# Kernel tuning notes

Hardware: AMD Instinct MI355X
Metric: run time of the kernel (lower is better)

The kernel has to match this reference:

```python
import jax, jax.numpy as jnp
import numpy as np

D, H, DFF = 1024, 16, 4096
B, T, S = 2, 2048, 2048
DK = D // H
EPS = 1e-5


def _linear(x, W, b):
    # torch nn.Linear: x @ W.T + b
    return jnp.einsum('bsd,od->bso', x, W) + b


def _mha(q_in, k_in, v_in, mask, Wq, bq, Wk, bk, Wv, bv, Wo, bo):
    Bq = q_in.shape[0]
    Q = _linear(q_in, Wq, bq).reshape(Bq, -1, H, DK)
    K = _linear(k_in, Wk, bk).reshape(Bq, -1, H, DK)
    V = _linear(v_in, Wv, bv).reshape(Bq, -1, H, DK)
    scores = jnp.einsum('bqhd,bkhd->bhqk', Q, K) / jnp.sqrt(jnp.float32(DK))
    if mask is not None:
        scores = jnp.where(mask[:, None, :, :] == 0, jnp.float32(-1e9), scores)
    attn = jax.nn.softmax(scores, axis=-1)
    ctx = jnp.einsum('bhqk,bkhd->bqhd', attn, V).reshape(Bq, -1, D)
    return _linear(ctx, Wo, bo)


def _ln(x, g, b):
    mu = jnp.mean(x, axis=-1, keepdims=True)
    var = jnp.mean((x - mu) ** 2, axis=-1, keepdims=True)
    return (x - mu) * jax.lax.rsqrt(var + EPS) * g + b


def setup_inputs() -> dict:
    key = jax.random.key(0)
    ks = jax.random.split(key, 24)
    sc = 0.02
    d = {
        'x': jax.random.normal(ks[0], (B, T, D), jnp.float32),
        'encoder_output': jax.random.normal(ks[1], (B, S, D), jnp.float32),
        'src_mask': jnp.ones((B, T, S), jnp.int32),
        'tgt_mask': jnp.tril(jnp.ones((T, T), jnp.int32))[None].repeat(B, axis=0),
    }
    i = 2
    for p in ['sa', 'ca']:
        for w in ['Wq', 'Wk', 'Wv', 'Wo']:
            d[f'{p}_{w}'] = jax.random.normal(ks[i], (D, D), jnp.float32) * sc; i += 1
            d[f'{p}_b{w[1]}'] = jnp.zeros((D,), jnp.float32)
    d['ff_W1'] = jax.random.normal(ks[i], (DFF, D), jnp.float32) * sc; i += 1
    d['ff_b1'] = jnp.zeros((DFF,), jnp.float32)
    d['ff_W2'] = jax.random.normal(ks[i], (D, DFF), jnp.float32) * sc; i += 1
    d['ff_b2'] = jnp.zeros((D,), jnp.float32)
    for n in ['ln1', 'ln2', 'ln3']:
        d[f'{n}_g'] = jnp.ones((D,), jnp.float32)
        d[f'{n}_b'] = jnp.zeros((D,), jnp.float32)
    return d


def reference(x, encoder_output, src_mask, tgt_mask,
              sa_Wq, sa_bq, sa_Wk, sa_bk, sa_Wv, sa_bv, sa_Wo, sa_bo,
              ca_Wq, ca_bq, ca_Wk, ca_bk, ca_Wv, ca_bv, ca_Wo, ca_bo,
              ff_W1, ff_b1, ff_W2, ff_b2,
              ln1_g, ln1_b, ln2_g, ln2_b, ln3_g, ln3_b):
    sa = _mha(x, x, x, tgt_mask, sa_Wq, sa_bq, sa_Wk, sa_bk, sa_Wv, sa_bv, sa_Wo, sa_bo)
    x = _ln(x + sa, ln1_g, ln1_b)
    ca = _mha(x, encoder_output, encoder_output, src_mask,
              ca_Wq, ca_bq, ca_Wk, ca_bk, ca_Wv, ca_bv, ca_Wo, ca_bo)
    x = _ln(x + ca, ln2_g, ln2_b)
    ff = _linear(jax.nn.relu(_linear(x, ff_W1, ff_b1)), ff_W2, ff_b2)
    return _ln(x + ff, ln3_g, ln3_b)
```

## Files before the change

### kernel.cpp

```cpp
#include <hip/hip_runtime.h>
#include <hip/hip_bf16.h>
#include <stdint.h>


#define D_MODEL 1024
#define NH      16
#define DKH     64
#define DFF_    4096
#define BB      2
#define TT      2048
#define SS      2048

typedef unsigned short ushort_t;
typedef __attribute__((ext_vector_type(8))) short short8;
typedef __attribute__((ext_vector_type(4))) float floatx4;
typedef __attribute__((ext_vector_type(16))) float floatx16;
typedef __attribute__((ext_vector_type(2))) unsigned int uint2v;

__device__ __forceinline__ float bf2f(ushort_t u) {
    union { unsigned int i; float f; } v; v.i = ((unsigned int)u) << 16; return v.f;
}
__device__ __forceinline__ ushort_t f2bf(float f) {
    union { float f; unsigned int i; } v; v.f = f;
    unsigned int r = v.i + 0x7fffu + ((v.i >> 16) & 1u);
    return (ushort_t)(r >> 16);
}
__device__ __forceinline__ unsigned int cvtpk_bf16(float a, float b) {
    unsigned int r;
    asm("v_cvt_pk_bf16_f32 %0, %1, %2" : "=v"(r) : "v"(a), "v"(b));
    return r;
}
__device__ __forceinline__ void gl16(const void* g, void* l) {
    __builtin_amdgcn_global_load_lds(
        (const __attribute__((address_space(1))) unsigned int*)g,
        (__attribute__((address_space(3))) unsigned int*)l, 16, 0, 0);
}

__global__ void probe_dtype(const unsigned int* __restrict__ g, int* __restrict__ flag)
{
    if (threadIdx.x == 0) *flag = (g[0] == 0x3F800000u) ? 1 : 0;
}

struct CvtSeg { const void* src; ushort_t* dst; int n; };
struct CvtArgs { CvtSeg seg[16]; };

__global__ __launch_bounds__(256)
void cvt_bf16(CvtArgs a, const int* __restrict__ flag)
{
    const CvtSeg s = a.seg[blockIdx.y];
    const int i = (blockIdx.x * 256 + threadIdx.x) * 8;
    if (i >= s.n) return;
    if (*flag) {
        const float* sp = (const float*)s.src;
        const float4 x = *(const float4*)(sp + i);
        const float4 y = *(const float4*)(sp + i + 4);
        union { uint4 v; ushort_t u[8]; } o;
        o.u[0] = f2bf(x.x); o.u[1] = f2bf(x.y); o.u[2] = f2bf(x.z); o.u[3] = f2bf(x.w);
        o.u[4] = f2bf(y.x); o.u[5] = f2bf(y.y); o.u[6] = f2bf(y.z); o.u[7] = f2bf(y.w);
        *(uint4*)(s.dst + i) = o.v;
    } else {
        *(uint4*)(s.dst + i) = *(const uint4*)((const ushort_t*)s.src + i);
    }
}

template<int BN>
__global__ __launch_bounds__(256)
void gemm_bt(const ushort_t* __restrict__ A, const ushort_t* __restrict__ W,
             const ushort_t* __restrict__ bias, ushort_t* __restrict__ C,
             int M, int N, int K, int do_relu)
{
    constexpr int MI = (BN == 128) ? 4 : 2;
    __shared__ ushort_t Alds[2][128 * 32];
    __shared__ ushort_t Blds[2][BN * 32];
    const int t  = threadIdx.x;
    const int l  = t & 63;
    const int w  = t >> 6;
    const int wm = (BN == 128) ? (w >> 1) : w;
    const int wn = (BN == 128) ? (w & 1) : 0;
    const int mbase = (BN == 128) ? wm * 64 : wm * 32;
    const int lm = l & 15, lq = l >> 4;
    const int m0 = blockIdx.y * 128, n0 = blockIdx.x * BN;

    floatx4 acc[MI][4];
#pragma unroll
    for (int i = 0; i < MI; i++)
#pragma unroll
        for (int j = 0; j < 4; j++) acc[i][j] = (floatx4){0.f, 0.f, 0.f, 0.f};

    const int row = t >> 2;
    const int kc  = (t & 3) * 8;
    const ushort_t* Ag = A + (long)(m0 + row) * K + kc;
    const ushort_t* Bg = W + (long)(n0 + row) * K + kc;

#define GSTAGE(BUF, K0)                                                     \
    do {                                                                    \
        gl16(Ag + (K0),           Alds[BUF] + t * 8);                       \
        gl16(Ag + 64l * K + (K0), Alds[BUF] + 2048 + t * 8);                \
        gl16(Bg + (K0),           Blds[BUF] + t * 8);                       \
        if (BN == 128) gl16(Bg + 64l * K + (K0), Blds[BUF] + 2048 + t * 8); \
    } while (0)

#define GCOMP(BUF)                                                          \
    do {                                                                    \
        short8 af[MI], bfr[4];                                              \
        _Pragma("unroll")                                                   \
        for (int i = 0; i < MI; i++)                                        \
            af[i] = *(const short8*)(Alds[BUF] + (mbase + i * 16 + lm) * 32 + lq * 8); \
        _Pragma("unroll")                                                   \
        for (int j = 0; j < 4; j++)                                         \
            bfr[j] = *(const short8*)(Blds[BUF] + (wn * 64 + j * 16 + lm) * 32 + lq * 8); \
        _Pragma("unroll")                                                   \
        for (int i = 0; i < MI; i++)                                        \
            _Pragma("unroll")                                               \
            for (int j = 0; j < 4; j++)                                     \
                acc[i][j] = __builtin_amdgcn_mfma_f32_16x16x32_bf16(af[i], bfr[j], acc[i][j], 0, 0, 0); \
    } while (0)

    GSTAGE(0, 0);
    __syncthreads();
    for (int k0 = 0; k0 < K; k0 += 64) {
        GSTAGE(1, k0 + 32);
        GCOMP(0);
        __syncthreads();
        if (k0 + 64 < K) GSTAGE(0, k0 + 64);
        GCOMP(1);
        __syncthreads();
    }
#undef GSTAGE
#undef GCOMP

#pragma unroll
    for (int j = 0; j < 4; j++) {
        const int n = n0 + wn * 64 + j * 16 + lm;
        const float bv = bf2f(bias[n]);
#pragma unroll
        for (int i = 0; i < MI; i++) {
            const int mr = m0 + mbase + i * 16 + lq * 4;
#pragma unroll
            for (int r = 0; r < 4; r++) {
                float v = acc[i][j][r] + bv;
                if (do_relu) v = fmaxf(v, 0.f);
                C[(long)(mr + r) * N + n] = f2bf(v);
            }
        }
    }
}

__global__ __launch_bounds__(256)
void transpose_v(const ushort_t* __restrict__ V, int vs,
                 ushort_t* __restrict__ Vt)
{
    __shared__ ushort_t tile[64 * 66];
    const int t  = threadIdx.x;
    const int h  = blockIdx.x;
    const int s0 = blockIdx.y * 64;
    const int b  = blockIdx.z;
#pragma unroll
    for (int i = 0; i < 2; i++) {
        const int tt = i * 256 + t;
        const int s = tt >> 3, c = tt & 7;
        union { uint4 v; ushort_t u[8]; } val;
        val.v = *(const uint4*)(V + (long)(b * SS + s0 + s) * vs + h * 64 + c * 8);
#pragma unroll
        for (int j = 0; j < 8; j++) tile[s * 66 + c * 8 + j] = val.u[j];
    }
    __syncthreads();
#pragma unroll
    for (int i = 0; i < 2; i++) {
        const int tt = i * 256 + t;
        const int d = tt >> 3, c = tt & 7;
        union { uint4 v; ushort_t u[8]; } out;
#pragma unroll
        for (int j = 0; j < 8; j++) out.u[j] = tile[(c * 8 + j) * 66 + d];
        *(uint4*)(Vt + (long)((b * NH + h) * DKH + d) * SS + s0 + c * 8) = out.v;
    }
}

#define LP 72
__global__ __launch_bounds__(256)
void flash_attn(const ushort_t* __restrict__ Qp, int qs,
                const ushort_t* __restrict__ Kp, int ks,
                const ushort_t* __restrict__ Vt,
                ushort_t* __restrict__ Ob, int causal)
{
    __shared__ __align__(16) ushort_t lds[2 * 2 * 64 * LP];
    const int t  = threadIdx.x;
    const int l  = t & 63;
    const int w  = t >> 6;
    const int wq = w >> 1;
    const int wk = w & 1;
    const int qt = blockIdx.x;
    const int bh = blockIdx.y;
    const int b  = bh >> 4;
    const int h  = bh & 15;
    const int ln = l & 31;
    const int hi = l >> 5;

    const long qrow = (long)(b * TT + qt * 64 + wq * 32 + ln) * qs + h * DKH;
    short8 qf[4];
#pragma unroll
    for (int c = 0; c < 4; c++)
        qf[c] = *(const short8*)(Qp + qrow + c * 16 + hi * 8);

    const floatx16 zero16 = {0.f,0.f,0.f,0.f,0.f,0.f,0.f,0.f,0.f,0.f,0.f,0.f,0.f,0.f,0.f,0.f};
    floatx16 o0 = zero16;
    floatx16 o1 = zero16;
    float l_part = 0.f;

    const float C1 = 0.18033688011112042f;
    const float C0 = -11.541560327111708f;

    const int nkt  = causal ? (qt + 1) : (SS / 64);
    const int srow = t >> 3;
    const int sc   = (t & 7) * 8;

    const ushort_t* Kg2 = Kp + ((long)b * SS + srow) * ks + h * DKH + sc;
    const ushort_t* Vg2 = Vt + ((long)bh * DKH + srow) * SS + sc;

    uint4 kv0 = *(const uint4*)(Kg2);
    uint4 kv1 = *(const uint4*)(Kg2 + 32l * ks);
    uint4 vv0 = *(const uint4*)(Vg2);
    uint4 vv1 = *(const uint4*)(Vg2 + 32l * SS);
    Kg2 += 64l * ks; Vg2 += 64;

    const int q_abs = qt * 64 + wq * 32 + ln;
    const bool dw = causal && (wq == 0) && (wk == 1);

#define FA_TILE(BUF, KT)                                                      \
  do {                                                                        \
    ushort_t* Kl = lds + (BUF) * (2 * 64 * LP);                               \
    ushort_t* Vl = Kl + 64 * LP;                                              \
    *(uint4*)(Kl + srow * LP + sc)        = kv0;              \
    *(uint4*)(Kl + (srow + 32) * LP + sc) = kv1;                              \
    *(uint4*)(Vl + srow * LP + sc)        = vv0;              \
    *(uint4*)(Vl + (srow + 32) * LP + sc) = vv1;                              \
    __syncthreads();                        \
    if ((KT) + 1 < nkt) {                   \
        kv0 = *(const uint4*)(Kg2);                                           \
        kv1 = *(const uint4*)(Kg2 + 32l * ks);                                \
        vv0 = *(const uint4*)(Vg2);                                           \
        vv1 = *(const uint4*)(Vg2 + 32l * SS);                                \
        Kg2 += 64l * ks; Vg2 += 64;                                           \
    }                                                                         \
    if (!(dw && (KT) == qt)) {                                                \
          \
        floatx16 z = zero16;                                                  \
        __builtin_amdgcn_s_setprio(1);                                        \
        _Pragma("unroll")                                                     \
        for (int c = 0; c < 4; c++) {                                         \
            const short8 ak = *(const short8*)(Kl + (wk * 32 + ln) * LP + c * 16 + hi * 8); \
            z = __builtin_amdgcn_mfma_f32_32x32x16_bf16(ak, qf[c], z, 0, 0, 0); \
        }                                                                     \
        __builtin_amdgcn_s_setprio(0);                                        \
        float pf[16];                                                         \
        if (causal && (KT) == qt) {            \
            const int kbase = (KT) * 64 + wk * 32 + 4 * hi;                   \
            _Pragma("unroll")                                                 \
            for (int r = 0; r < 16; r++) {                                    \
                float pe = __builtin_amdgcn_exp2f(__builtin_fmaf(z[r], C1, C0)); \
                const int key = kbase + (r & 3) + 8 * (r >> 2);               \
                if (key > q_abs) pe = 0.f;                                    \
                pf[r] = pe;                                                   \
                l_part += pe;                                                 \
            }                                                                 \
        } else {                                           \
            _Pragma("unroll")                                                 \
            for (int r = 0; r < 16; r++) {                                    \
                const float pe = __builtin_amdgcn_exp2f(__builtin_fmaf(z[r], C1, C0)); \
                pf[r] = pe;                                                   \
                l_part += pe;                                                 \
            }                                                                 \
        }                                                                     \
                           \
        unsigned int cv[8];                                                   \
        _Pragma("unroll")                                                     \
        for (int i = 0; i < 8; i++) cv[i] = cvtpk_bf16(pf[2 * i], pf[2 * i + 1]); \
        short8 pa[2];                                                         \
        _Pragma("unroll")                                                     \
        for (int kc = 0; kc < 2; kc++) {                                      \
            uint2v r02 = __builtin_amdgcn_permlane32_swap(cv[4 * kc + 0], cv[4 * kc + 2], false, false); \
            uint2v r13 = __builtin_amdgcn_permlane32_swap(cv[4 * kc + 1], cv[4 * kc + 3], false, false); \
            union { unsigned int u[4]; short8 s; } pu;                        \
            pu.u[0] = r02[0]; pu.u[1] = r13[0]; pu.u[2] = r02[1]; pu.u[3] = r13[1]; \
            pa[kc] = pu.s;                                                    \
        }                                                                     \
          \
        __builtin_amdgcn_s_setprio(1);                                        \
        _Pragma("unroll")                                                     \
        for (int kc = 0; kc < 2; kc++) {                                      \
            const int koff = wk * 32 + kc * 16 + hi * 8;                      \
            const short8 v0 = *(const short8*)(Vl + ln * LP + koff);          \
            const short8 v1 = *(const short8*)(Vl + (32 + ln) * LP + koff);   \
            o0 = __builtin_amdgcn_mfma_f32_32x32x16_bf16(pa[kc], v0, o0, 0, 0, 0); \
            o1 = __builtin_amdgcn_mfma_f32_32x32x16_bf16(pa[kc], v1, o1, 0, 0, 0); \
        }                                                                     \
        __builtin_amdgcn_s_setprio(0);                                        \
    }                                                                         \
  } while (0)

    int kt = 0;
    for (; kt + 1 < nkt; kt += 2) {
        FA_TILE(0, kt);
        FA_TILE(1, kt + 1);
    }
    if (kt < nkt) FA_TILE(0, kt);
#undef FA_TILE

    l_part += __shfl_xor(l_part, 32, 64);

    __syncthreads();
    float* fl = (float*)lds;
    if (wk == 1) {
#pragma unroll
        for (int r = 0; r < 16; r++) {
            const int qr = (r & 3) + 8 * (r >> 2) + 4 * hi;
            fl[wq * 2048 + qr * 64 + ln]      = o0[r];
            fl[wq * 2048 + qr * 64 + 32 + ln] = o1[r];
        }
        if (hi == 0) fl[4096 + wq * 32 + ln] = l_part;
    }
    __syncthreads();
    if (wk == 0) {
        const float L = l_part + fl[4096 + wq * 32 + ln];
#pragma unroll
        for (int r = 0; r < 16; r++) {
            const int qr = (r & 3) + 8 * (r >> 2) + 4 * hi;
            const float ov0 = o0[r] + fl[wq * 2048 + qr * 64 + ln];
            const float ov1 = o1[r] + fl[wq * 2048 + qr * 64 + 32 + ln];
            const float inv = 1.0f / fmaxf(__shfl(L, qr, 64), 1e-30f);
            const long orow = (long)(b * TT + qt * 64 + wq * 32 + qr) * D_MODEL + h * DKH;
            Ob[orow + ln]      = f2bf(ov0 * inv);
            Ob[orow + 32 + ln] = f2bf(ov1 * inv);
        }
    }
}

__device__ __forceinline__ void ln_core(const ushort_t* X, const ushort_t* Rs,
                                        const ushort_t* G, const ushort_t* Bt,
                                        int row, int t, float* red, float y[4], long* baseOut)
{
    const long base = (long)row * D_MODEL + t * 4;
    const ushort4 xv = *(const ushort4*)(X + base);
    const ushort4 rv = *(const ushort4*)(Rs + base);
    const float v0 = bf2f(xv.x) + bf2f(rv.x);
    const float v1 = bf2f(xv.y) + bf2f(rv.y);
    const float v2 = bf2f(xv.z) + bf2f(rv.z);
    const float v3 = bf2f(xv.w) + bf2f(rv.w);
    float s  = v0 + v1 + v2 + v3;
    float sq = v0 * v0 + v1 * v1 + v2 * v2 + v3 * v3;
#pragma unroll
    for (int off = 1; off < 64; off <<= 1) {
        s  += __shfl_xor(s, off, 64);
        sq += __shfl_xor(sq, off, 64);
    }
    if ((t & 63) == 0) { red[t >> 6] = s; red[4 + (t >> 6)] = sq; }
    __syncthreads();
    const float S  = red[0] + red[1] + red[2] + red[3];
    const float SQ = red[4] + red[5] + red[6] + red[7];
    const float mean = S * (1.0f / D_MODEL);
    const float var  = SQ * (1.0f / D_MODEL) - mean * mean;
    const float rstd = rsqrtf(var + 1e-5f);
    const ushort4 gv = *(const ushort4*)(G + t * 4);
    const ushort4 bv = *(const ushort4*)(Bt + t * 4);
    y[0] = (v0 - mean) * rstd * bf2f(gv.x) + bf2f(bv.x);
    y[1] = (v1 - mean) * rstd * bf2f(gv.y) + bf2f(bv.y);
    y[2] = (v2 - mean) * rstd * bf2f(gv.z) + bf2f(bv.z);
    y[3] = (v3 - mean) * rstd * bf2f(gv.w) + bf2f(bv.w);
    *baseOut = base;
}

__global__ __launch_bounds__(256)
void ln_residual(const ushort_t* __restrict__ X, const ushort_t* __restrict__ Rs,
                 const ushort_t* __restrict__ G, const ushort_t* __restrict__ Bt,
                 ushort_t* __restrict__ Y)
{
    __shared__ float red[8];
    float y[4]; long base;
    ln_core(X, Rs, G, Bt, blockIdx.x, threadIdx.x, red, y, &base);
    ushort4 yv = { f2bf(y[0]), f2bf(y[1]), f2bf(y[2]), f2bf(y[3]) };
    *(ushort4*)(Y + base) = yv;
}

__global__ __launch_bounds__(256)
void ln_residual_out(const ushort_t* __restrict__ X, const ushort_t* __restrict__ Rs,
                     const ushort_t* __restrict__ G, const ushort_t* __restrict__ Bt,
                     void* __restrict__ Y, const int* __restrict__ flag)
{
    __shared__ float red[8];
    float y[4]; long base;
    ln_core(X, Rs, G, Bt, blockIdx.x, threadIdx.x, red, y, &base);
    if (*flag) {
        float4 o = { y[0], y[1], y[2], y[3] };
        *(float4*)((float*)Y + base) = o;
    } else {
        ushort4 yv = { f2bf(y[0]), f2bf(y[1]), f2bf(y[2]), f2bf(y[3]) };
        *(ushort4*)((ushort_t*)Y + base) = yv;
    }
}

extern "C" void kernel_launch(void* const* d_in, const int* in_sizes, int n_in,
                              void* d_out, int out_size, void* d_ws, size_t ws_size,
                              hipStream_t stream)
{
    (void)in_sizes; (void)n_in; (void)out_size; (void)ws_size;
    ushort_t* ws = (ushort_t*)d_ws;
    int* flag = (int*)d_ws;
    const size_t MEG = 1024 * 1024;

    ushort_t* cx    = ws + 512;
    ushort_t* cenc  = cx    + 4 * MEG;
    ushort_t* Wslot = cenc  + 4 * MEG;
    ushort_t* csm   = Wslot + 4 * MEG;
    ushort_t* P0    = csm   + 32768;
    ushort_t* bQKV  = P0;
    ushort_t* bQ2   = P0;
    ushort_t* bKV   = P0 + 4 * MEG;
    ushort_t* bVt   = P0 + 12 * MEG;
    ushort_t* bF    = P0;
    ushort_t* bC    = P0 + 16 * MEG;
    ushort_t* ffW2c = bC;
    ushort_t* bO    = P0 + 20 * MEG;
    ushort_t* bX1   = P0 + 24 * MEG;
    ushort_t* bX2   = P0 + 28 * MEG;

    const dim3 blk(256);
    const int M = BB * TT;

    probe_dtype<<<1, 64, 0, stream>>>((const unsigned int*)d_in[24], flag);

    {
        CvtArgs a = {};
        a.seg[0] = { d_in[0],  cx,              (int)(4 * MEG) };
        a.seg[1] = { d_in[1],  cenc,            (int)(4 * MEG) };
        a.seg[2] = { d_in[4],  Wslot + 0 * MEG, (int)MEG };
        a.seg[3] = { d_in[6],  Wslot + 1 * MEG, (int)MEG };
        a.seg[4] = { d_in[8],  Wslot + 2 * MEG, (int)MEG };
        a.seg[5] = { d_in[10], Wslot + 3 * MEG, (int)MEG };
        cvt_bf16<<<dim3(2048, 6), blk, 0, stream>>>(a, flag);
    }
    ushort_t* b_saQKV = csm;
    ushort_t* b_saO   = csm + 3072;
    ushort_t* b_caQ   = csm + 4096;
    ushort_t* b_caKV  = csm + 5120;
    ushort_t* b_caO   = csm + 7168;
    ushort_t* b_ff1   = csm + 8192;
    ushort_t* b_ff2   = csm + 12288;
    ushort_t* lnp     = csm + 13312;
    {
        CvtArgs a = {};
        a.seg[0]  = { d_in[5],  b_saQKV,        1024 };
        a.seg[1]  = { d_in[7],  b_saQKV + 1024, 1024 };
        a.seg[2]  = { d_in[9],  b_saQKV + 2048, 1024 };
        a.seg[3]  = { d_in[11], b_saO,          1024 };
        a.seg[4]  = { d_in[13], b_caQ,          1024 };
        a.seg[5]  = { d_in[15], b_caKV,         1024 };
        a.seg[6]  = { d_in[17], b_caKV + 1024,  1024 };
        a.seg[7]  = { d_in[19], b_caO,          1024 };
        a.seg[8]  = { d_in[21], b_ff1,          4096 };
        a.seg[9]  = { d_in[23], b_ff2,          1024 };
        for (int i = 0; i < 6; i++)
            a.seg[10 + i] = { d_in[24 + i], lnp + i * 1024, 1024 };
        cvt_bf16<<<dim3(2, 16), blk, 0, stream>>>(a, flag);
    }

    gemm_bt<128><<<dim3(24, 32), blk, 0, stream>>>(cx, Wslot, b_saQKV, bQKV, M, 3072, 1024, 0);
    transpose_v<<<dim3(16, 32, 2), blk, 0, stream>>>(bQKV + 2048, 3072, bVt);
    flash_attn<<<dim3(32, 32), blk, 0, stream>>>(bQKV, 3072, bQKV + 1024, 3072, bVt, bC, 1);
    gemm_bt<64><<<dim3(16, 32), blk, 0, stream>>>(bC, Wslot + 3 * MEG, b_saO, bO, M, 1024, 1024, 0);
    {
        CvtArgs a = {};
        a.seg[0] = { d_in[12], Wslot + 0 * MEG, (int)MEG };
        a.seg[1] = { d_in[14], Wslot + 1 * MEG, (int)MEG };
        a.seg[2] = { d_in[16], Wslot + 2 * MEG, (int)MEG };
        a.seg[3] = { d_in[18], Wslot + 3 * MEG, (int)MEG };
        cvt_bf16<<<dim3(512, 4), blk, 0, stream>>>(a, flag);
    }
    ln_residual<<<dim3(M), blk, 0, stream>>>(cx, bO, lnp, lnp + 1024, bX1);

    gemm_bt<64><<<dim3(16, 32), blk, 0, stream>>>(bX1, Wslot, b_caQ, bQ2, M, 1024, 1024, 0);
    gemm_bt<128><<<dim3(16, 32), blk, 0, stream>>>(cenc, Wslot + 1 * MEG, b_caKV, bKV, M, 2048, 1024, 0);
    transpose_v<<<dim3(16, 32, 2), blk, 0, stream>>>(bKV + 1024, 2048, bVt);
    flash_attn<<<dim3(32, 32), blk, 0, stream>>>(bQ2, 1024, bKV, 2048, bVt, bC, 0);
    gemm_bt<64><<<dim3(16, 32), blk, 0, stream>>>(bC, Wslot + 3 * MEG, b_caO, bO, M, 1024, 1024, 0);
    {
        CvtArgs a = {};
        a.seg[0] = { d_in[20], Wslot, (int)(4 * MEG) };
        a.seg[1] = { d_in[22], ffW2c, (int)(4 * MEG) };
        cvt_bf16<<<dim3(2048, 2), blk, 0, stream>>>(a, flag);
    }
    ln_residual<<<dim3(M), blk, 0, stream>>>(bX1, bO, lnp + 2048, lnp + 3072, bX2);

    gemm_bt<128><<<dim3(32, 32), blk, 0, stream>>>(bX2, Wslot, b_ff1, bF, M, DFF_, 1024, 1);
    gemm_bt<64><<<dim3(16, 32), blk, 0, stream>>>(bF, ffW2c, b_ff2, bO, M, 1024, DFF_, 0);
    ln_residual_out<<<dim3(M), blk, 0, stream>>>(bX2, bO, lnp + 4096, lnp + 5120, d_out, flag);
}
```

Baseline: 608.3 us.

## Triple-buffer GEMM loads with vmcnt waits and XCD-aware block remapping

The GEMM moves from a double-buffered LDS pipeline with __syncthreads to a three-stage ring buffer. Explicit s_waitcnt vmcnt counts and raw s_barrier calls keep two tile loads in flight while one tile is computed. Both the GEMM and flash-attention kernels also remap block IDs so consecutive IDs, which round-robin across the 8 XCDs, land on neighbouring tiles within one XCD to improve L2 reuse. The cost is 50% more LDS per GEMM block, which can lower occupancy, and redundant clamped loads on the last iterations.

```diff
diff --git a/kernel.cpp b/kernel.cpp
--- a/kernel.cpp
+++ b/kernel.cpp
@@ -70,8 +70,8 @@
              int M, int N, int K, int do_relu)
 {
     constexpr int MI = (BN == 128) ? 4 : 2;
-    __shared__ ushort_t Alds[2][128 * 32];
-    __shared__ ushort_t Blds[2][BN * 32];
+    __shared__ ushort_t Alds[3][128 * 32];
+    __shared__ ushort_t Blds[3][BN * 32];
     const int t  = threadIdx.x;
     const int l  = t & 63;
     const int w  = t >> 6;
@@ -79,7 +79,14 @@
     const int wn = (BN == 128) ? (w & 1) : 0;
     const int mbase = (BN == 128) ? wm * 64 : wm * 32;
     const int lm = l & 15, lq = l >> 4;
-    const int m0 = blockIdx.y * 128, n0 = blockIdx.x * BN;
+
+    const int gx  = gridDim.x;
+    const int nwg = gx * gridDim.y;
+    int bid = blockIdx.y * gx + blockIdx.x;
+    bid = (bid & 7) * (nwg >> 3) + (bid >> 3);
+    const int bx = bid % gx;
+    const int by = bid / gx;
+    const int m0 = by * 128, n0 = bx * BN;
 
     floatx4 acc[MI][4];
 #pragma unroll
@@ -116,15 +123,22 @@
                 acc[i][j] = __builtin_amdgcn_mfma_f32_16x16x32_bf16(af[i], bfr[j], acc[i][j], 0, 0, 0); \
     } while (0)
 
+    const int nk = K >> 5;
     GSTAGE(0, 0);
-    __syncthreads();
-    for (int k0 = 0; k0 < K; k0 += 64) {
-        GSTAGE(1, k0 + 32);
-        GCOMP(0);
-        __syncthreads();
-        if (k0 + 64 < K) GSTAGE(0, k0 + 64);
-        GCOMP(1);
-        __syncthreads();
+    GSTAGE(1, 32);
+    GSTAGE(2, 64);
+    int buf = 0;
+    for (int k = 0; k < nk; ++k) {
+        if constexpr (BN == 128) asm volatile("s_waitcnt vmcnt(8)" ::: "memory");
+        else                     asm volatile("s_waitcnt vmcnt(6)" ::: "memory");
+        __builtin_amdgcn_sched_barrier(0);
+        __builtin_amdgcn_s_barrier();
+        GCOMP(buf);
+        __builtin_amdgcn_s_barrier();
+        int kn = k + 3;
+        if (kn > nk - 1) kn = nk - 1;
+        GSTAGE(buf, kn * 32);
+        buf = (buf == 2) ? 0 : buf + 1;
     }
 #undef GSTAGE
 #undef GCOMP
@@ -189,8 +203,11 @@
     const int w  = t >> 6;
     const int wq = w >> 1;
     const int wk = w & 1;
-    const int qt = blockIdx.x;
-    const int bh = blockIdx.y;
+
+    int bid = blockIdx.y * 32 + blockIdx.x;
+    bid = (bid & 7) * 128 + (bid >> 3);
+    const int qt = bid & 31;
+    const int bh = bid >> 5;
     const int b  = bh >> 4;
     const int h  = bh & 15;
     const int ln = l & 31;
```

New measurement: 565.4 us. 7.1% less time.
